# Optimization experiments

Hardware: AMD Instinct MI355X
Metric: run time of the kernel (lower is better)

The kernel has to match this reference:

```python
import jax, jax.numpy as jnp
import numpy as np


def _dct_basis(N):
    # X[k] = 2 * sum_n x[n] * cos(pi * k * (2n+1) / (2N))  -- matches the
    # flip+concat+rfft+twiddle path of the torch module (unnormalized DCT-II x2).
    k = jnp.arange(N, dtype=jnp.float32)[:, None]
    n = jnp.arange(N, dtype=jnp.float32)[None, :]
    return 2.0 * jnp.cos(jnp.pi * k * (2.0 * n + 1.0) / (2.0 * N))  # (K, N)


def _dct2(x):
    B, C, H, W = x.shape
    Bw = _dct_basis(W)
    Bh = _dct_basis(H)
    x = jnp.einsum('bchw,kw->bchk', x, Bw)  # DCT along W
    x = jnp.einsum('bchw,kh->bckw', x, Bh)  # DCT along H
    return x


def _conv3x3(x, w, b):
    y = jax.lax.conv_general_dilated(x, w, window_strides=(1, 1), padding='SAME',
                                     dimension_numbers=('NCHW', 'OIHW', 'NCHW'))
    return y + b[None, :, None, None]


def _bn(x, g, be, m, v):
    # inference-mode BatchNorm2d, eps = 1e-5
    inv = jax.lax.rsqrt(v + 1e-5)
    return (x - m[None, :, None, None]) * (g * inv)[None, :, None, None] + be[None, :, None, None]


def setup_inputs() -> dict:
    key = jax.random.key(0)
    ks = jax.random.split(key, 16)
    B, C, H, W = 32, 1, 224, 224
    mid, emb = 128, 256
    s = 0.05
    return {
        'x':  jax.random.normal(ks[0], (B, C, H, W), jnp.float32),
        'w1': jax.random.normal(ks[1], (64, C, 3, 3), jnp.float32) * s,
        'b1': jax.random.normal(ks[2], (64,), jnp.float32) * s,
        'g1': jax.random.uniform(ks[3], (64,), jnp.float32, 0.5, 1.5),
        'be1': jax.random.normal(ks[4], (64,), jnp.float32) * s,
        'm1': jax.random.normal(ks[5], (64,), jnp.float32) * s,
        'v1': jax.random.uniform(ks[6], (64,), jnp.float32, 0.5, 1.5),
        'w2': jax.random.normal(ks[7], (mid, 64, 3, 3), jnp.float32) * s,
        'b2': jax.random.normal(ks[8], (mid,), jnp.float32) * s,
        'g2': jax.random.uniform(ks[9], (mid,), jnp.float32, 0.5, 1.5),
        'be2': jax.random.normal(ks[10], (mid,), jnp.float32) * s,
        'm2': jax.random.normal(ks[11], (mid,), jnp.float32) * s,
        'v2': jax.random.uniform(ks[12], (mid,), jnp.float32, 0.5, 1.5),
        'wp': jax.random.normal(ks[13], (emb, mid), jnp.float32) * s,
        'bp': jax.random.normal(ks[14], (emb,), jnp.float32) * s,
    }


def reference(x, w1, b1, g1, be1, m1, v1, w2, b2, g2, be2, m2, v2, wp, bp):
    USE_TOPK = 0.5
    X = _dct2(x)                                   # (B, 1, H, W)
    B, C, H, W = X.shape
    k_h, k_w = int(H * USE_TOPK), int(W * USE_TOPK)
    mask = jnp.zeros((H, W), X.dtype).at[:k_h, :k_w].set(1.0)
    X = X * mask[None, None]
    h = jax.nn.relu(_bn(_conv3x3(X, w1, b1), g1, be1, m1, v1))
    h = jax.nn.relu(_bn(_conv3x3(h, w2, b2), g2, be2, m2, v2))
    h = jnp.mean(h, axis=(2, 3))                   # AdaptiveAvgPool2d((1,1)) -> (B, mid)
    return h @ wp.T + bp                           # (B, emb_dim)
```

## Files before the change

### kernel.cpp

```cpp
#include <hip/hip_runtime.h>
#include <math.h>


#define NPIX 224
#define KEEP 112
#define H1DIM 115
#define ADIM 114

typedef short bf16x8 __attribute__((ext_vector_type(8)));
typedef float f32x4  __attribute__((ext_vector_type(4)));

__device__ __forceinline__ unsigned short f2bf(float f) {
    unsigned int u = __float_as_uint(f);
    unsigned int r = (u + 0x7FFFu + ((u >> 16) & 1u)) >> 16;
    return (unsigned short)r;
}

__global__ __launch_bounds__(256) void prep_kernel(
    const float* __restrict__ w1, const float* __restrict__ b1,
    const float* __restrict__ g1, const float* __restrict__ be1,
    const float* __restrict__ m1, const float* __restrict__ v1,
    const float* __restrict__ w2,
    float* __restrict__ Bst, float* __restrict__ P,
    float* __restrict__ ws1, float* __restrict__ wb1,
    uint4* __restrict__ w2f) {
    int bx = blockIdx.x, tid = threadIdx.x;
    if (bx < 49) {
        int idx = bx * 256 + tid;
        if (idx < KEEP * KEEP) {
            int n = idx / KEEP, k = idx - n * KEEP;
            double ang = 3.14159265358979323846 * (double)k * (2.0 * n + 1.0) / (2.0 * NPIX);
            Bst[n * KEEP + k] = (float)(2.0 * cos(ang));
        }
    } else if (bx < 54) {
        __shared__ float c1s[64];
        if (tid < 64) {
            float sc = g1[tid] * rsqrtf(v1[tid] + 1e-5f);
            c1s[tid] = fmaxf((b1[tid] - m1[tid]) * sc + be1[tid], 0.f);
        }
        __syncthreads();
        int idx = (bx - 49) * 256 + tid;
        if (idx < 128 * 9) {
            int oc = idx / 9, tap = idx - oc * 9;
            float s = 0.f;
            for (int ic = 0; ic < 64; ++ic)
                s = fmaf(w2[((size_t)oc * 64 + ic) * 9 + tap], c1s[ic], s);
            P[idx] = s;
        }
    } else if (bx == 54) {
        if (tid < 64) {
            float sc = g1[tid] * rsqrtf(v1[tid] + 1e-5f);
            wb1[tid] = (b1[tid] - m1[tid]) * sc + be1[tid];
            for (int t = 0; t < 9; ++t) ws1[tid * 9 + t] = w1[tid * 9 + t] * sc;
        }
    } else {
        int j = (bx - 55) * 256 + tid;
        if (j < 9216) {
            int t = j >> 10;
            int r = j & 1023;
            int kc = (r >> 9) & 1;
            int g16 = (r >> 6) & 7;
            int lane = r & 63;
            int oc = g16 * 16 + (lane & 15);
            int ic0 = kc * 32 + (lane >> 4) * 8;
            union { unsigned short us[8]; uint4 v; } u;
#pragma unroll
            for (int q = 0; q < 8; ++q)
                u.us[q] = f2bf(w2[((size_t)oc * 64 + ic0 + q) * 9 + t]);
            w2f[j] = u.v;
        }
    }
}

__global__ __launch_bounds__(128) void dct_w_kernel(const float* __restrict__ x,
                                                    const float* __restrict__ Bst,
                                                    float* __restrict__ tmp1) {
    int blk = blockIdx.x;
    int tid = threadIdx.x;
    __shared__ float eo[2][4][112];
    const float* rows = x + (size_t)blk * 4 * NPIX;
    for (int i = tid; i < 448; i += 128) {
        int r = i / 112, n = i - r * 112;
        float a = rows[r * NPIX + n], bv = rows[r * NPIX + 223 - n];
        eo[0][r][n] = a + bv;
        eo[1][r][n] = a - bv;
    }
    __syncthreads();
    int kw = tid;
    if (kw >= KEEP) return;
    const float* eop = &eo[kw & 1][0][0];
    float a0 = 0.f, a1 = 0.f, a2 = 0.f, a3 = 0.f;
    for (int n = 0; n < 112; ++n) {
        float bs = Bst[n * KEEP + kw];
        a0 = fmaf(eop[n], bs, a0);
        a1 = fmaf(eop[112 + n], bs, a1);
        a2 = fmaf(eop[224 + n], bs, a2);
        a3 = fmaf(eop[336 + n], bs, a3);
    }
    size_t base = (size_t)blk * 4 * KEEP + kw;
    tmp1[base] = a0; tmp1[base + 112] = a1; tmp1[base + 224] = a2; tmp1[base + 336] = a3;
}

__global__ __launch_bounds__(512) void dct_h_kernel(const float* __restrict__ tmp1,
                                                    const float* __restrict__ Bst,
                                                    float* __restrict__ Xd) {
    int kq = blockIdx.x, b = blockIdx.y;
    int tid = threadIdx.x;
    int kw = tid & 127, sub = tid >> 7;
    __shared__ float ps[3][4][112];
    const int kh0 = kq * 4;
    float a0 = 0.f, a1 = 0.f, a2 = 0.f, a3 = 0.f;
    if (kw < KEEP) {
        const float* t = tmp1 + (size_t)b * NPIX * KEEP + kw;
        for (int h = sub * 28; h < sub * 28 + 28; ++h) {
            float lo = t[(size_t)h * KEEP];
            float hi = t[(size_t)(223 - h) * KEEP];
            float e = lo + hi, o = lo - hi;
            const float* bs = Bst + h * KEEP + kh0;
            a0 = fmaf(e, bs[0], a0);
            a1 = fmaf(o, bs[1], a1);
            a2 = fmaf(e, bs[2], a2);
            a3 = fmaf(o, bs[3], a3);
        }
        if (sub) {
            ps[sub - 1][0][kw] = a0; ps[sub - 1][1][kw] = a1;
            ps[sub - 1][2][kw] = a2; ps[sub - 1][3][kw] = a3;
        }
    }
    __syncthreads();
    if (sub == 0 && kw < KEEP) {
        a0 += ps[0][0][kw] + ps[1][0][kw] + ps[2][0][kw];
        a1 += ps[0][1][kw] + ps[1][1][kw] + ps[2][1][kw];
        a2 += ps[0][2][kw] + ps[1][2][kw] + ps[2][2][kw];
        a3 += ps[0][3][kw] + ps[1][3][kw] + ps[2][3][kw];
        float* X = Xd + ((size_t)b * KEEP + kh0) * KEEP + kw;
        X[0] = a0; X[112] = a1; X[224] = a2; X[336] = a3;
    }
}

__global__ __launch_bounds__(256) void conv1_kernel(const float* __restrict__ Xd,
                                                    const float* __restrict__ ws1,
                                                    const float* __restrict__ wb1,
                                                    unsigned short* __restrict__ h1c) {
    const int r = blockIdx.y, b = blockIdx.z;
    const int c0 = blockIdx.x * 32;
    const int tid = threadIdx.x;
    __shared__ float xs[3][36];
    __shared__ float wsm[8][73];
    __shared__ float wbs[64];
    const float* X = Xd + (size_t)b * KEEP * KEEP;
    for (int i = tid; i < 102; i += 256) {
        int dr = i / 34, dc = i - dr * 34;
        int rr = r - 1 + dr, cc = c0 - 1 + dc;
        xs[dr][dc] = ((unsigned)rr < (unsigned)KEEP && (unsigned)cc < (unsigned)KEEP)
                         ? X[rr * KEEP + cc] : 0.f;
    }
    for (int i = tid; i < 576; i += 256) {
        int ic = i / 9, t = i - ic * 9;
        wsm[ic >> 3][(ic & 7) * 9 + t] = ws1[i];
    }
    if (tid < 64) wbs[tid] = wb1[tid];
    __syncthreads();

    const int px = tid >> 3, icg = tid & 7;
    const int c = c0 + px;
    float xv[9];
#pragma unroll
    for (int ky = 0; ky < 3; ++ky)
#pragma unroll
        for (int kx = 0; kx < 3; ++kx) xv[ky * 3 + kx] = xs[ky][px + kx];

    union { unsigned short us[8]; uint4 v; } u;
#pragma unroll
    for (int j = 0; j < 8; ++j) {
        float s = wbs[icg * 8 + j];
#pragma unroll
        for (int t = 0; t < 9; ++t) s = fmaf(xv[t], wsm[icg][j * 9 + t], s);
        u.us[j] = f2bf(fmaxf(s, 0.f));
    }
    if (c < H1DIM) {
        unsigned short* dst = h1c + (((size_t)b * H1DIM + r) * H1DIM + c) * 64 + icg * 8;
        *reinterpret_cast<uint4*>(dst) = u.v;
    }
}

__global__ __launch_bounds__(512, 4) void conv2_mfma_kernel(
    const unsigned short* __restrict__ h1c, const uint4* __restrict__ w2f,
    const float* __restrict__ b2, const float* __restrict__ g2,
    const float* __restrict__ be2, const float* __restrict__ m2,
    const float* __restrict__ v2, float* __restrict__ partial) {
    const int tc = blockIdx.x, tr = blockIdx.y, b = blockIdx.z;
    const int r0 = tr * 16, c0 = tc * 16;
    const int tid = threadIdx.x;
    const int lane = tid & 63, w = tid >> 6;
    const int mg = w & 3, og = w >> 2;
    const int l15 = lane & 15, h4 = lane >> 4;

    __shared__ unsigned short At[324 * 64];

    const unsigned short* __restrict__ h1b = h1c + (size_t)b * (H1DIM * H1DIM * 64);
    for (int e = tid; e < 2592; e += 512) {
        int px = e >> 3, gi = e & 7;
        int pr = px / 18, pc = px - pr * 18;
        int gr = r0 + pr - 1, gc = c0 + pc - 1;
        uint4 v = make_uint4(0u, 0u, 0u, 0u);
        if ((unsigned)gr < (unsigned)H1DIM && (unsigned)gc < (unsigned)H1DIM)
            v = *reinterpret_cast<const uint4*>(h1b + ((size_t)(gr * H1DIM + gc)) * 64 + gi * 8);
        *reinterpret_cast<uint4*>(&At[px * 64 + ((gi * 8) ^ ((px & 7) << 3))]) = v;
    }
    __syncthreads();

    f32x4 acc[4][4];
#pragma unroll
    for (int f = 0; f < 4; ++f)
#pragma unroll
        for (int n = 0; n < 4; ++n) acc[f][n] = (f32x4){0.f, 0.f, 0.f, 0.f};

    const int flim = ADIM - (r0 + 4 * mg);
    if (flim > 0) {
        bf16x8 Bf[2][4];
#define LOADB(buf, t, kc)                                                               \
    {                                                                                   \
        const uint4* bp = w2f + (size_t)(((t) * 2 + (kc)) * 8 + og * 4) * 64 + lane;    \
        Bf[buf][0] = *reinterpret_cast<const bf16x8*>(bp);                              \
        Bf[buf][1] = *reinterpret_cast<const bf16x8*>(bp + 64);                         \
        Bf[buf][2] = *reinterpret_cast<const bf16x8*>(bp + 128);                        \
        Bf[buf][3] = *reinterpret_cast<const bf16x8*>(bp + 192);                        \
    }
        LOADB(0, 0, 0);
#pragma unroll
        for (int s = 0; s < 18; ++s) {
            const int kc = s / 9, t = s - 9 * kc;
            if (s + 1 < 18) {
                const int nk = (s + 1) / 9, nt = (s + 1) - 9 * nk;
                LOADB((s + 1) & 1, nt, nk);
            }
            const int ky = t / 3, kx = t - 3 * ky;
#pragma unroll
            for (int f = 0; f < 4; ++f) {
                if (f < flim) {
                    const int px = (4 * mg + f + ky) * 18 + l15 + kx;
                    const bf16x8 a = *reinterpret_cast<const bf16x8*>(
                        &At[px * 64 + ((kc * 32 + h4 * 8) ^ ((px & 7) << 3))]);
                    acc[f][0] = __builtin_amdgcn_mfma_f32_16x16x32_bf16(a, Bf[s & 1][0], acc[f][0], 0, 0, 0);
                    acc[f][1] = __builtin_amdgcn_mfma_f32_16x16x32_bf16(a, Bf[s & 1][1], acc[f][1], 0, 0, 0);
                    acc[f][2] = __builtin_amdgcn_mfma_f32_16x16x32_bf16(a, Bf[s & 1][2], acc[f][2], 0, 0, 0);
                    acc[f][3] = __builtin_amdgcn_mfma_f32_16x16x32_bf16(a, Bf[s & 1][3], acc[f][3], 0, 0, 0);
                }
            }
        }
#undef LOADB
    }

    const int tile = tr * 8 + tc;
    float* pslice = partial + (((size_t)b * 64 + tile) * 4 + mg) * 128;
#pragma unroll
    for (int n = 0; n < 4; ++n) {
        int oc = og * 64 + n * 16 + l15;
        float sc = g2[oc] * rsqrtf(v2[oc] + 1e-5f);
        float bias = b2[oc] - m2[oc];
        float add = be2[oc];
        float s = 0.f;
#pragma unroll
        for (int f = 0; f < 4; ++f) {
            int row = r0 + 4 * mg + f;
            bool rok = row < ADIM;
#pragma unroll
            for (int i = 0; i < 4; ++i) {
                int col = c0 + (h4 << 2) + i;
                float v = fmaxf(fmaf(acc[f][n][i] + bias, sc, add), 0.f);
                s += (rok && col < ADIM) ? v : 0.f;
            }
        }
        s += __shfl_xor(s, 16);
        s += __shfl_xor(s, 32);
        if (lane < 16) pslice[oc] = s;
    }
}

__global__ __launch_bounds__(256) void reduce_mean_kernel(
    const float* __restrict__ partial, const float* __restrict__ P,
    const float* __restrict__ b2, const float* __restrict__ g2,
    const float* __restrict__ be2, const float* __restrict__ m2,
    const float* __restrict__ v2, float* __restrict__ mean) {
    int b = blockIdx.x, ocg = blockIdx.y;
    int tid = threadIdx.x;
    int ocl = tid & 15, jq = tid >> 4;
    int oc = ocg * 16 + ocl;
    const float* pb = partial + (size_t)b * 256 * 128 + oc;
    float s = 0.f;
#pragma unroll
    for (int jj = 0; jj < 16; ++jj) s += pb[(size_t)(jq * 16 + jj) * 128];
    __shared__ float red[16][17];
    red[jq][ocl] = s;
    __syncthreads();
    if (jq == 0) {
        float tot = 0.f;
#pragma unroll
        for (int k = 0; k < 16; ++k) tot += red[k][ocl];

        float p[9];
#pragma unroll
        for (int t = 0; t < 9; ++t) p[t] = P[oc * 9 + t];

        float Sall = p[0] + p[1] + p[2] + p[3] + p[4] + p[5] + p[6] + p[7] + p[8];
        float Stop = p[3] + p[4] + p[5] + p[6] + p[7] + p[8];
        float Sbot = p[0] + p[1] + p[2] + p[3] + p[4] + p[5];
        float Sleft  = p[1] + p[2] + p[4] + p[5] + p[7] + p[8];
        float Sright = p[0] + p[1] + p[3] + p[4] + p[6] + p[7];
        float Ctr = p[3] + p[4] + p[6] + p[7];
        float Cbl = p[1] + p[2] + p[4] + p[5];
        float Cbr = p[0] + p[1] + p[3] + p[4];

        float bias = b2[oc], mm = m2[oc], bb = be2[oc];
        float sc = g2[oc] * rsqrtf(v2[oc] + 1e-5f);
#define VALOF(S) fmaxf(((bias) + (S) - (mm)) * (sc) + (bb), 0.f)
        float cs = 36515.f * VALOF(Sall) + 109.f * VALOF(Stop) + 109.f * VALOF(Sleft)
                 + 222.f * VALOF(Sbot) + 222.f * VALOF(Sright)
                 + VALOF(Ctr) + VALOF(Cbl) + VALOF(Cbr);
#undef VALOF
        mean[b * 128 + oc] = (tot + cs) * (1.f / (224.f * 224.f));
    }
}

__global__ __launch_bounds__(256) void final_linear_kernel(const float* __restrict__ mean,
                                                           const float* __restrict__ wp,
                                                           const float* __restrict__ bp,
                                                           float* __restrict__ out) {
    int b = blockIdx.x, e = threadIdx.x;
    __shared__ float mrow[128];
    if (threadIdx.x < 128) mrow[threadIdx.x] = mean[b * 128 + threadIdx.x];
    __syncthreads();
    const float4* wr = reinterpret_cast<const float4*>(wp + (size_t)e * 128);
    float s = bp[e];
#pragma unroll 8
    for (int c = 0; c < 32; ++c) {
        float4 wv = wr[c];
        s = fmaf(mrow[4 * c], wv.x, s);
        s = fmaf(mrow[4 * c + 1], wv.y, s);
        s = fmaf(mrow[4 * c + 2], wv.z, s);
        s = fmaf(mrow[4 * c + 3], wv.w, s);
    }
    out[(size_t)b * 256 + e] = s;
}

extern "C" void kernel_launch(void* const* d_in, const int* in_sizes, int n_in,
                              void* d_out, int out_size, void* d_ws, size_t ws_size,
                              hipStream_t stream) {
    const float* x   = (const float*)d_in[0];
    const float* w1  = (const float*)d_in[1];
    const float* b1  = (const float*)d_in[2];
    const float* g1  = (const float*)d_in[3];
    const float* be1 = (const float*)d_in[4];
    const float* m1  = (const float*)d_in[5];
    const float* v1  = (const float*)d_in[6];
    const float* w2  = (const float*)d_in[7];
    const float* b2  = (const float*)d_in[8];
    const float* g2  = (const float*)d_in[9];
    const float* be2 = (const float*)d_in[10];
    const float* m2  = (const float*)d_in[11];
    const float* v2  = (const float*)d_in[12];
    const float* wp  = (const float*)d_in[13];
    const float* bp  = (const float*)d_in[14];
    float* out = (float*)d_out;

    float* ws = (float*)d_ws;
    size_t off = 0;
    float* Bst  = ws + off; off += (size_t)KEEP * KEEP;
    float* tmp1 = ws + off; off += (size_t)32 * NPIX * KEEP;
    float* Xd   = ws + off; off += (size_t)32 * KEEP * KEEP;
    float* P    = ws + off; off += 128 * 9;
    float* ws1  = ws + off; off += 64 * 9;
    float* wb1  = ws + off; off += 64;
    uint4* w2f  = (uint4*)(ws + off); off += (size_t)9216 * 4;
    float* part = ws + off; off += (size_t)32 * 256 * 128;
    float* mean = ws + off; off += 32 * 128;
    unsigned short* h1c = (unsigned short*)(ws + off);
    off += (size_t)32 * H1DIM * H1DIM * 64 / 2;

    if (ws_size < off * sizeof(float)) return;

    prep_kernel<<<dim3(91), dim3(256), 0, stream>>>(w1, b1, g1, be1, m1, v1, w2,
                                                    Bst, P, ws1, wb1, w2f);
    dct_w_kernel<<<dim3(32 * 56), dim3(128), 0, stream>>>(x, Bst, tmp1);
    dct_h_kernel<<<dim3(28, 32), dim3(512), 0, stream>>>(tmp1, Bst, Xd);
    conv1_kernel<<<dim3(4, H1DIM, 32), dim3(256), 0, stream>>>(Xd, ws1, wb1, h1c);
    conv2_mfma_kernel<<<dim3(8, 8, 32), dim3(512), 0, stream>>>(
        h1c, w2f, b2, g2, be2, m2, v2, part);
    reduce_mean_kernel<<<dim3(32, 8), dim3(256), 0, stream>>>(part, P, b2, g2, be2, m2, v2, mean);
    final_linear_kernel<<<dim3(32), dim3(256), 0, stream>>>(mean, wp, bp, out);
}
```

Before: 154.5 us.

## Switch conv2 MFMA from 16x16x32 to 32x32x16 tiles with repacked weights

Conv2's implicit GEMM now uses 32x32x16 bf16 MFMA instructions, with each wave computing two 32-pixel by 32-channel tiles per output group instead of sixteen 16x16 tiles. The weight prepack is rewritten to match the new B-fragment layout (K chunks of 16, 32 output channels per group). This halves the number of MFMA issues and B-fragment loads per K step and raises arithmetic density per LDS read. The explicit double-buffering of B fragments is dropped, the epilogue index mapping is rewritten for the 32x32 accumulator layout, and row-validity masking becomes coarser (per pair of rows).

```diff
diff --git a/kernel.cpp b/kernel.cpp
--- a/kernel.cpp
+++ b/kernel.cpp
@@ -9,6 +9,7 @@
 
 typedef short bf16x8 __attribute__((ext_vector_type(8)));
 typedef float f32x4  __attribute__((ext_vector_type(4)));
+typedef float f32x16 __attribute__((ext_vector_type(16)));
 
 __device__ __forceinline__ unsigned short f2bf(float f) {
     unsigned int u = __float_as_uint(f);
@@ -56,17 +57,15 @@
     } else {
         int j = (bx - 55) * 256 + tid;
         if (j < 9216) {
-            int t = j >> 10;
-            int r = j & 1023;
-            int kc = (r >> 9) & 1;
-            int g16 = (r >> 6) & 7;
-            int lane = r & 63;
-            int oc = g16 * 16 + (lane & 15);
-            int ic0 = kc * 32 + (lane >> 4) * 8;
+            int q = j >> 6, lane = j & 63;
+            int tap = q / 16, rem = q & 15;
+            int kc = rem >> 2, g32 = rem & 3;
+            int oc = g32 * 32 + (lane & 31);
+            int ic0 = kc * 16 + (lane >> 5) * 8;
             union { unsigned short us[8]; uint4 v; } u;
 #pragma unroll
-            for (int q = 0; q < 8; ++q)
-                u.us[q] = f2bf(w2[((size_t)oc * 64 + ic0 + q) * 9 + t]);
+            for (int t_ = 0; t_ < 8; ++t_)
+                u.us[t_] = f2bf(w2[((size_t)oc * 64 + ic0 + t_) * 9 + tap]);
             w2f[j] = u.v;
         }
     }
@@ -194,7 +193,6 @@
     const int tid = threadIdx.x;
     const int lane = tid & 63, w = tid >> 6;
     const int mg = w & 3, og = w >> 2;
-    const int l15 = lane & 15, h4 = lane >> 4;
 
     __shared__ unsigned short At[324 * 64];
 
@@ -210,71 +208,64 @@
     }
     __syncthreads();
 
-    f32x4 acc[4][4];
-#pragma unroll
-    for (int f = 0; f < 4; ++f)
-#pragma unroll
-        for (int n = 0; n < 4; ++n) acc[f][n] = (f32x4){0.f, 0.f, 0.f, 0.f};
-
-    const int flim = ADIM - (r0 + 4 * mg);
-    if (flim > 0) {
-        bf16x8 Bf[2][4];
-#define LOADB(buf, t, kc)                                                               \
-    {                                                                                   \
-        const uint4* bp = w2f + (size_t)(((t) * 2 + (kc)) * 8 + og * 4) * 64 + lane;    \
-        Bf[buf][0] = *reinterpret_cast<const bf16x8*>(bp);                              \
-        Bf[buf][1] = *reinterpret_cast<const bf16x8*>(bp + 64);                         \
-        Bf[buf][2] = *reinterpret_cast<const bf16x8*>(bp + 128);                        \
-        Bf[buf][3] = *reinterpret_cast<const bf16x8*>(bp + 192);                        \
-    }
-        LOADB(0, 0, 0);
-#pragma unroll
-        for (int s = 0; s < 18; ++s) {
-            const int kc = s / 9, t = s - 9 * kc;
-            if (s + 1 < 18) {
-                const int nk = (s + 1) / 9, nt = (s + 1) - 9 * nk;
-                LOADB((s + 1) & 1, nt, nk);
-            }
-            const int ky = t / 3, kx = t - 3 * ky;
-#pragma unroll
-            for (int f = 0; f < 4; ++f) {
-                if (f < flim) {
-                    const int px = (4 * mg + f + ky) * 18 + l15 + kx;
+    f32x16 acc[2][2];
+#pragma unroll
+    for (int F = 0; F < 2; ++F)
+#pragma unroll
+        for (int N = 0; N < 2; ++N)
+#pragma unroll
+            for (int i = 0; i < 16; ++i) acc[F][N][i] = 0.f;
+
+    const int flim2 = ADIM - r0 - 4 * mg;
+    if (flim2 > 0) {
+        const int rowbase = 4 * mg + ((lane & 31) >> 4);
+        const int colbase = lane & 15;
+        const int khalf = (lane >> 5) * 8;
+#pragma unroll
+        for (int s = 0; s < 36; ++s) {
+            const int tap = s >> 2, kc = s & 3;
+            const int ky = tap / 3, kx = tap - 3 * ky;
+            const int icoff = kc * 16 + khalf;
+            const bf16x8* bq = reinterpret_cast<const bf16x8*>(
+                w2f + (size_t)(((tap * 4 + kc) * 4) + og * 2) * 64 + lane);
+            const bf16x8 b0 = bq[0];
+            const bf16x8 b1 = bq[64];
+#pragma unroll
+            for (int F = 0; F < 2; ++F) {
+                if (2 * F < flim2) {
+                    const int px = (rowbase + 2 * F + ky) * 18 + colbase + kx;
                     const bf16x8 a = *reinterpret_cast<const bf16x8*>(
-                        &At[px * 64 + ((kc * 32 + h4 * 8) ^ ((px & 7) << 3))]);
-                    acc[f][0] = __builtin_amdgcn_mfma_f32_16x16x32_bf16(a, Bf[s & 1][0], acc[f][0], 0, 0, 0);
-                    acc[f][1] = __builtin_amdgcn_mfma_f32_16x16x32_bf16(a, Bf[s & 1][1], acc[f][1], 0, 0, 0);
-                    acc[f][2] = __builtin_amdgcn_mfma_f32_16x16x32_bf16(a, Bf[s & 1][2], acc[f][2], 0, 0, 0);
-                    acc[f][3] = __builtin_amdgcn_mfma_f32_16x16x32_bf16(a, Bf[s & 1][3], acc[f][3], 0, 0, 0);
+                        &At[px * 64 + (icoff ^ ((px & 7) << 3))]);
+                    acc[F][0] = __builtin_amdgcn_mfma_f32_32x32x16_bf16(a, b0, acc[F][0], 0, 0, 0);
+                    acc[F][1] = __builtin_amdgcn_mfma_f32_32x32x16_bf16(a, b1, acc[F][1], 0, 0, 0);
                 }
             }
         }
-#undef LOADB
     }
 
     const int tile = tr * 8 + tc;
     float* pslice = partial + (((size_t)b * 64 + tile) * 4 + mg) * 128;
 #pragma unroll
-    for (int n = 0; n < 4; ++n) {
-        int oc = og * 64 + n * 16 + l15;
+    for (int N = 0; N < 2; ++N) {
+        int oc = og * 64 + N * 32 + (lane & 31);
         float sc = g2[oc] * rsqrtf(v2[oc] + 1e-5f);
         float bias = b2[oc] - m2[oc];
         float add = be2[oc];
         float s = 0.f;
 #pragma unroll
-        for (int f = 0; f < 4; ++f) {
-            int row = r0 + 4 * mg + f;
-            bool rok = row < ADIM;
-#pragma unroll
-            for (int i = 0; i < 4; ++i) {
-                int col = c0 + (h4 << 2) + i;
-                float v = fmaxf(fmaf(acc[f][n][i] + bias, sc, add), 0.f);
-                s += (rok && col < ADIM) ? v : 0.f;
+        for (int F = 0; F < 2; ++F) {
+#pragma unroll
+            for (int rg = 0; rg < 16; ++rg) {
+                int m = (rg & 3) + 8 * (rg >> 2) + 4 * (lane >> 5);
+                int p = ((2 * mg + F) << 5) + m;
+                int row = r0 + (p >> 4);
+                int col = c0 + (p & 15);
+                float v = fmaxf(fmaf(acc[F][N][rg] + bias, sc, add), 0.f);
+                s += (row < ADIM && col < ADIM) ? v : 0.f;
             }
         }
-        s += __shfl_xor(s, 16);
         s += __shfl_xor(s, 32);
-        if (lane < 16) pslice[oc] = s;
+        if (lane < 32) pslice[og * 64 + N * 32 + lane] = s;
     }
 }
 
```

Measured after the change: 135.9 us. 12.0% less time.
